# Kernel optimization log

Measured on AMD Instinct MI355X. Metric: run time of the kernel, lower is better.

## Reference

```python
import jax, jax.numpy as jnp
import numpy as np

E, T = 8, 256          # n_experts, chunk length
IN, OUT = 1024, 1024   # input_size, output_size
D1, D2 = 32, 32        # nearest factors of IN
DO1, DO2 = 32, 32      # nearest factors of OUT
B, L = 8, 2048
LOSS_COEF = 1e-5


def setup_inputs() -> dict:
    key = jax.random.key(0)
    ks = jax.random.split(key, 12)
    eyeE = lambda d, k: (jnp.broadcast_to(jnp.eye(d, dtype=jnp.float32), (E, d, d))
                         + 0.01 * jax.random.normal(k, (E, d, d), jnp.float32))
    return {
        "x": jax.random.normal(ks[0], (B, L, IN), jnp.float32),
        "w_gate": 0.02 * jax.random.normal(ks[1], (IN, E), jnp.float32),
        "weight": 0.02 * jax.random.normal(ks[2], (E, OUT, IN), jnp.float32),
        "bias": 0.02 * jax.random.normal(ks[3], (E, OUT), jnp.float32),
        "res_weight": 0.02 * jax.random.normal(ks[4], (OUT, IN), jnp.float32),
        "res_bias": 0.02 * jax.random.normal(ks[5], (1, OUT), jnp.float32),
        "curve1_in": eyeE(D1, ks[6]),
        "curve2_in": eyeE(D2, ks[7]),
        "curve1_out": eyeE(DO1, ks[8]),
        "curve2_out": eyeE(DO2, ks[9]),
        "curve1_bias": eyeE(DO1, ks[10]),
        "curve2_bias": eyeE(DO2, ks[11]),
    }


def _cv_squared(v):
    v = v.astype(jnp.float32)
    return jnp.var(v, ddof=1) / (jnp.mean(v) ** 2 + 1e-10)


def reference(x, w_gate, weight, bias, res_weight, res_bias,
              curve1_in, curve2_in, curve1_out, curve2_out,
              curve1_bias, curve2_bias):
    Bx, Lx, d = x.shape
    N = Lx // T
    BN = Bx * N
    xr = x.reshape(BN, T, d)

    # --- gating (eval mode, ties_merging forces k = n_experts -> plain softmax) ---
    logits = xr.mean(axis=1) @ w_gate            # [BN, E]
    gates = jax.nn.softmax(logits, axis=1)        # [BN, E]
    load = (gates > 0).sum(axis=0).astype(jnp.float32)
    importance = gates.sum(axis=0)
    loss = (_cv_squared(importance) + _cv_squared(load)) * LOSS_COEF

    # --- roll gates by one segment, keeping each sample's first chunk (detached) ---
    e_first = jax.lax.stop_gradient(gates.reshape(Bx, N, E)[:, 0])
    g = jnp.roll(gates, 1, axis=0).reshape(Bx, N, E)
    g = g.at[:, 0].set(e_first).reshape(BN, E)

    # --- Kronecker curve-factored expert weight merge ---
    rw = (weight - res_weight).reshape(E, DO1, DO2, D1, D2)
    rw = jnp.einsum('bij,bjklm->biklm', curve1_out, rw)
    rw = jnp.einsum('bik,bjklm->bjilm', curve2_out, rw)
    rw = jnp.einsum('bil,bjklm->bjkim', curve1_in, rw)
    rw = jnp.einsum('bim,bjklm->bjkli', curve2_in, rw)
    rw = rw.reshape(E, OUT, IN)
    expert_weights = res_weight + jnp.einsum('be,eoi->boi', g, rw)  # [BN, O, I]

    y = jnp.einsum('bij,bkj->bik', xr, expert_weights)  # [BN, T, O]

    # --- curve-factored expert bias merge ---
    rb = (bias - res_bias).reshape(E, DO1, DO2)
    rb = jnp.einsum('bki,bij->bkj', curve1_bias, rb)      # [E, DO1, DO2]
    rb = jnp.einsum('bkj,bij->bik', curve2_bias, rb)      # [E, DO1, DO2]
    rb = rb.reshape(E, OUT)
    expert_bias = res_bias + jnp.einsum('be,eo->bo', g, rb)  # [BN, O]

    y = (y + expert_bias[:, None, :]).reshape(Bx, Lx, OUT)
    return y, loss
```

## Files before the change

kernel.cpp:

```cpp
#include <hip/hip_runtime.h>
#include <cstdint>

typedef __bf16 bf16x8 __attribute__((ext_vector_type(8)));
typedef float  f32x4  __attribute__((ext_vector_type(4)));
typedef unsigned int u32x4 __attribute__((ext_vector_type(4)));
using u16 = unsigned short;

struct alignas(8) u16x4 { u16 x, y, z, w; };

__device__ __forceinline__ u16 f2bf(float f) {
  unsigned u = __builtin_bit_cast(unsigned, f);
  u = (u + 0x7FFFu + ((u >> 16) & 1u)) >> 16;
  return (u16)u;
}
__device__ __forceinline__ float bf2f(u16 u) {
  unsigned v = ((unsigned)u) << 16;
  return __builtin_bit_cast(float, v);
}

static constexpr size_t OFF_XBF  = 0;
static constexpr size_t OFF_EW   = 33554432;
static constexpr size_t OFF_T2   = 33554432;
static constexpr size_t OFF_PM   = 67108864;
static constexpr size_t OFF_RW   = 167772160;
static constexpr size_t OFF_LG   = 201326592;
static constexpr size_t OFF_G    = 201588736;
static constexpr size_t OFF_RB   = 201592832;
static constexpr size_t WS_NEED  = 201887744;

__global__ __launch_bounds__(256) void k_means(const float* __restrict__ x,
                                               float* __restrict__ pm,
                                               u16* __restrict__ xbf) {
  int b = blockIdx.x, q = blockIdx.y, tid = threadIdx.x;
  const float* xb = x + (size_t)b * 262144 + (size_t)q * 16384 + tid * 4;
  u16* xo = xbf + (size_t)b * 262144 + (size_t)q * 16384 + tid * 4;
  float s0 = 0.f, s1 = 0.f, s2 = 0.f, s3 = 0.f;
#pragma unroll
  for (int t = 0; t < 16; ++t) {
    float4 v = *(const float4*)(xb + t * 1024);
    s0 += v.x; s1 += v.y; s2 += v.z; s3 += v.w;
    u16x4 o; o.x = f2bf(v.x); o.y = f2bf(v.y); o.z = f2bf(v.z); o.w = f2bf(v.w);
    *(u16x4*)(xo + t * 1024) = o;
  }
  float4 sv; sv.x = s0; sv.y = s1; sv.z = s2; sv.w = s3;
  *(float4*)(pm + ((size_t)b * 16 + q) * 1024 + tid * 4) = sv;
}

__global__ __launch_bounds__(256) void k_redlogits(const float* __restrict__ pm,
                                                   const float* __restrict__ w_gate,
                                                   float* __restrict__ logits) {
  __shared__ float red[4][8];
  int b = blockIdx.x, tid = threadIdx.x;
  const float* p = pm + (size_t)b * 16384 + tid * 4;
  float4 s = {0.f, 0.f, 0.f, 0.f};
#pragma unroll
  for (int q = 0; q < 16; ++q) {
    float4 v = *(const float4*)(p + q * 1024);
    s.x += v.x; s.y += v.y; s.z += v.z; s.w += v.w;
  }
  int i0 = tid * 4;
  float acc[8];
#pragma unroll
  for (int e = 0; e < 8; ++e) {
    acc[e] = s.x * w_gate[(i0 + 0) * 8 + e] + s.y * w_gate[(i0 + 1) * 8 + e]
           + s.z * w_gate[(i0 + 2) * 8 + e] + s.w * w_gate[(i0 + 3) * 8 + e];
  }
#pragma unroll
  for (int off = 32; off >= 1; off >>= 1)
#pragma unroll
    for (int e = 0; e < 8; ++e) acc[e] += __shfl_down(acc[e], off, 64);
  int wv = tid >> 6;
  if ((tid & 63) == 0)
#pragma unroll
    for (int e = 0; e < 8; ++e) red[wv][e] = acc[e];
  __syncthreads();
  if (tid < 8)
    logits[b * 8 + tid] =
        (red[0][tid] + red[1][tid] + red[2][tid] + red[3][tid]) * (1.f / 256.f);
}

__global__ __launch_bounds__(256) void k_mergeA(const float* __restrict__ W,
                                                const float* __restrict__ R,
                                                const float* __restrict__ c1o,
                                                const float* __restrict__ c2o,
                                                u16* __restrict__ T2t,
                                                const float* __restrict__ bias,
                                                const float* __restrict__ res_bias,
                                                const float* __restrict__ c1b,
                                                const float* __restrict__ c2b,
                                                float* __restrict__ rb) {
  int e = blockIdx.y, bx = blockIdx.x, tid = threadIdx.x;
  if (bx == 128) {
    __shared__ float rb0[32][33], rb1[32][33], m1b[32][32], m2b[32][32];
    for (int idx = tid; idx < 1024; idx += 256) {
      int i = idx >> 5, j = idx & 31;
      rb0[i][j] = bias[e * 1024 + idx] - res_bias[idx];
      m1b[i][j] = c1b[e * 1024 + idx];
      m2b[i][j] = c2b[e * 1024 + idx];
    }
    __syncthreads();
    for (int idx = tid; idx < 1024; idx += 256) {
      int p = idx >> 5, j = idx & 31;
      float s = 0.f;
#pragma unroll
      for (int i = 0; i < 32; ++i) s += m1b[p][i] * rb0[i][j];
      rb1[p][j] = s;
    }
    __syncthreads();
    for (int idx = tid; idx < 1024; idx += 256) {
      int p = idx >> 5, q = idx & 31;
      float s = 0.f;
#pragma unroll
      for (int j = 0; j < 32; ++j) s += m2b[q][j] * rb1[p][j];
      rb[e * 1024 + idx] = s;
    }
    return;
  }
  __shared__ float dw[8 * 1024];
  __shared__ float m1[1024], m2[1024];
  int c0 = bx * 8;
  const float* We = W + (size_t)e * 1048576;
  for (int idx = tid; idx < 1024; idx += 256) {
    m1[idx] = c1o[e * 1024 + idx];
    m2[idx] = c2o[e * 1024 + idx];
  }
  {
    int r = tid >> 1, h = (tid & 1) * 4;
#pragma unroll
    for (int i = 0; i < 8; ++i) {
      int row = r + i * 128;
      const float4 wv = *(const float4*)(We + (size_t)row * 1024 + c0 + h);
      const float4 rv = *(const float4*)(R + (size_t)row * 1024 + c0 + h);
      dw[(h + 0) * 1024 + row] = wv.x - rv.x;
      dw[(h + 1) * 1024 + row] = wv.y - rv.y;
      dw[(h + 2) * 1024 + row] = wv.z - rv.z;
      dw[(h + 3) * 1024 + row] = wv.w - rv.w;
    }
  }
  __syncthreads();
  int i1 = tid & 31, c = tid >> 5;
  const float* dwc = dw + c * 1024;
  float U[32];
#pragma unroll
  for (int k = 0; k < 32; ++k) U[k] = 0.f;
  for (int j = 0; j < 32; ++j) {
    float cj = m1[i1 * 32 + j];
    const float4* rowp = (const float4*)(dwc + j * 32);
#pragma unroll
    for (int k4 = 0; k4 < 8; ++k4) {
      float4 v = rowp[k4];
      U[k4 * 4 + 0] += cj * v.x; U[k4 * 4 + 1] += cj * v.y;
      U[k4 * 4 + 2] += cj * v.z; U[k4 * 4 + 3] += cj * v.w;
    }
  }
  u16* obase = T2t + (size_t)e * 1048576 + (size_t)(c0 + c) * 1024 + i1 * 32;
#pragma unroll
  for (int g4 = 0; g4 < 8; ++g4) {
    float s[4];
#pragma unroll
    for (int q = 0; q < 4; ++q) {
      const float4* m2r = (const float4*)(m2 + (g4 * 4 + q) * 32);
      float acc = 0.f;
#pragma unroll
      for (int k4 = 0; k4 < 8; ++k4) {
        float4 mv = m2r[k4];
        acc += mv.x * U[k4 * 4 + 0] + mv.y * U[k4 * 4 + 1]
             + mv.z * U[k4 * 4 + 2] + mv.w * U[k4 * 4 + 3];
      }
      s[q] = acc;
    }
    u16x4 o4; o4.x = f2bf(s[0]); o4.y = f2bf(s[1]); o4.z = f2bf(s[2]); o4.w = f2bf(s[3]);
    *(u16x4*)(obase + g4 * 4) = o4;
  }
}

__global__ __launch_bounds__(256) void k_mergeB(const u16* __restrict__ T2t,
                                                const float* __restrict__ c1i,
                                                const float* __restrict__ c2i,
                                                const float* __restrict__ R,
                                                u16* __restrict__ RWbf,
                                                const float* __restrict__ logits,
                                                float* __restrict__ g,
                                                float* __restrict__ loss_out) {
  int e = blockIdx.y, bx = blockIdx.x, tid = threadIdx.x;
  if (bx == 128) {
    if (e != 0) return;
    __shared__ float gates[64][8];
    __shared__ float imp[8];
    if (tid < 64) {
      float lg[8];
#pragma unroll
      for (int j = 0; j < 8; ++j) lg[j] = logits[tid * 8 + j];
      float mx = lg[0];
#pragma unroll
      for (int j = 1; j < 8; ++j) mx = fmaxf(mx, lg[j]);
      float s = 0.f, ex[8];
#pragma unroll
      for (int j = 0; j < 8; ++j) { ex[j] = expf(lg[j] - mx); s += ex[j]; }
      float inv = 1.f / s;
#pragma unroll
      for (int j = 0; j < 8; ++j) gates[tid][j] = ex[j] * inv;
    }
    __syncthreads();
    if (tid < 8) {
      float s = 0.f;
      for (int bb = 0; bb < 64; ++bb) s += gates[bb][tid];
      imp[tid] = s;
    }
    __syncthreads();
    if (tid == 0) {
      float mean = 0.f;
#pragma unroll
      for (int j = 0; j < 8; ++j) mean += imp[j];
      mean *= (1.f / 8.f);
      float var = 0.f;
#pragma unroll
      for (int j = 0; j < 8; ++j) { float d = imp[j] - mean; var += d * d; }
      var *= (1.f / 7.f);
      loss_out[0] = (var / (mean * mean + 1e-10f)) * 1e-5f;
    }
    __syncthreads();
    if (tid < 64) {
      int src = ((tid & 7) == 0) ? tid : tid - 1;
#pragma unroll
      for (int j = 0; j < 8; ++j) g[tid * 8 + j] = gates[src][j];
    }
    return;
  }
  __shared__ float t2[8 * 1024];
  __shared__ float m1[1024], m2[1024];
  int o0 = bx * 8;
  const u16* Te = T2t + (size_t)e * 1048576;
  for (int idx = tid; idx < 1024; idx += 256) {
    m1[idx] = c1i[e * 1024 + idx];
    m2[idx] = c2i[e * 1024 + idx];
  }
  {
    int r = tid >> 1, h = (tid & 1) * 4;
#pragma unroll
    for (int i = 0; i < 8; ++i) {
      int row = r + i * 128;
      const u16x4 tv = *(const u16x4*)(Te + (size_t)row * 1024 + o0 + h);
      t2[(h + 0) * 1024 + row] = bf2f(tv.x);
      t2[(h + 1) * 1024 + row] = bf2f(tv.y);
      t2[(h + 2) * 1024 + row] = bf2f(tv.z);
      t2[(h + 3) * 1024 + row] = bf2f(tv.w);
    }
  }
  __syncthreads();
  int i1 = tid & 31, oc = tid >> 5;
  const float* t2c = t2 + oc * 1024;
  float A[32];
#pragma unroll
  for (int m = 0; m < 32; ++m) A[m] = 0.f;
  for (int l = 0; l < 32; ++l) {
    float cl = m1[i1 * 32 + l];
    const float4* rowp = (const float4*)(t2c + l * 32);
#pragma unroll
    for (int m4 = 0; m4 < 8; ++m4) {
      float4 v = rowp[m4];
      A[m4 * 4 + 0] += cl * v.x; A[m4 * 4 + 1] += cl * v.y;
      A[m4 * 4 + 2] += cl * v.z; A[m4 * 4 + 3] += cl * v.w;
    }
  }
  const float* Rrow = R + (size_t)(o0 + oc) * 1024 + i1 * 32;
  u16* obase = RWbf + ((size_t)e * 1024 + o0 + oc) * 1024 + i1 * 32;
#pragma unroll
  for (int g4 = 0; g4 < 8; ++g4) {
    float s[4];
#pragma unroll
    for (int q = 0; q < 4; ++q) {
      const float4* m2r = (const float4*)(m2 + (g4 * 4 + q) * 32);
      float acc = Rrow[g4 * 4 + q];
#pragma unroll
      for (int m4 = 0; m4 < 8; ++m4) {
        float4 mv = m2r[m4];
        acc += mv.x * A[m4 * 4 + 0] + mv.y * A[m4 * 4 + 1]
             + mv.z * A[m4 * 4 + 2] + mv.w * A[m4 * 4 + 3];
      }
      s[q] = acc;
    }
    u16x4 o4; o4.x = f2bf(s[0]); o4.y = f2bf(s[1]); o4.z = f2bf(s[2]); o4.w = f2bf(s[3]);
    *(u16x4*)(obase + g4 * 4) = o4;
  }
}

__global__ __launch_bounds__(256) void k_combine(const u16* __restrict__ RWbf,
                                                 const float* __restrict__ g,
                                                 u16* __restrict__ EW) {
  __shared__ float gs[512];
  int blk = blockIdx.x, tid = threadIdx.x;
  for (int idx = tid; idx < 512; idx += 256) gs[idx] = g[idx];
  __syncthreads();
  int o = blk * 2 + (tid >> 7);
  int i0 = (tid & 127) * 8;
  float w[8][8];
#pragma unroll
  for (int e = 0; e < 8; ++e) {
    u32x4 v = *(const u32x4*)(RWbf + (size_t)e * 1048576 + (size_t)o * 1024 + i0);
#pragma unroll
    for (int h = 0; h < 4; ++h) {
      w[e][2 * h]     = __builtin_bit_cast(float, v[h] << 16);
      w[e][2 * h + 1] = __builtin_bit_cast(float, v[h] & 0xFFFF0000u);
    }
  }
  for (int b = 0; b < 64; ++b) {
    float a[8];
#pragma unroll
    for (int j = 0; j < 8; ++j) a[j] = 0.f;
#pragma unroll
    for (int e = 0; e < 8; ++e) {
      float ge = gs[b * 8 + e];
#pragma unroll
      for (int j = 0; j < 8; ++j) a[j] += ge * w[e][j];
    }
    u32x4 pk;
#pragma unroll
    for (int h = 0; h < 4; ++h)
      pk[h] = (unsigned)f2bf(a[2 * h]) | ((unsigned)f2bf(a[2 * h + 1]) << 16);
    *(u32x4*)(EW + (size_t)b * 1048576 + (size_t)o * 1024 + i0) = pk;
  }
}

__global__ __launch_bounds__(512) void k_gemm(const u16* __restrict__ Xb,
                                              const u16* __restrict__ EW,
                                              const float* __restrict__ rb,
                                              const float* __restrict__ res_b,
                                              const float* __restrict__ g,
                                              float* __restrict__ Y) {
  __shared__ alignas(16) u16 As[2][256 * 64];
  __shared__ alignas(16) u16 Bs[2][256 * 64];
  int hw = blockIdx.x;
  int xcd = hw & 7;
  int b  = xcd * 8 + (hw >> 5);
  int nt = (hw >> 3) & 3;
  int t0 = b * 256, o0 = nt * 256;
  int tid = threadIdx.x, lane = tid & 63, wv = tid >> 6;
  int wr = wv >> 2, wc = wv & 3;
  f32x4 acc[8][4] = {};
  const u16* aG = Xb + (size_t)t0 * 1024;
  const u16* bG = EW + (size_t)b * 1048576 + (size_t)o0 * 1024;
  int srow = tid >> 3;
  int kcol = (tid & 7) << 3;
  int lr = lane & 15;
  int sx = lr & 7;
  u32x4 la[4], lb[4];
#pragma unroll
  for (int iss = 0; iss < 4; ++iss) {
    int r = srow + iss * 64;
    la[iss] = *(const u32x4*)(aG + (size_t)r * 1024 + kcol);
    lb[iss] = *(const u32x4*)(bG + (size_t)r * 1024 + kcol);
  }
  for (int kt = 0; kt < 16; ++kt) {
    int cur = kt & 1;
#pragma unroll
    for (int iss = 0; iss < 4; ++iss) {
      int r = srow + iss * 64;
      int wcl = (((tid & 7) ^ (r & 7)) << 3);
      *(u32x4*)&As[cur][r * 64 + wcl] = la[iss];
      *(u32x4*)&Bs[cur][r * 64 + wcl] = lb[iss];
    }
    __syncthreads();
    if (kt < 15) {
      int k0n = (kt + 1) << 6;
#pragma unroll
      for (int iss = 0; iss < 4; ++iss) {
        int r = srow + iss * 64;
        la[iss] = *(const u32x4*)(aG + (size_t)r * 1024 + k0n + kcol);
        lb[iss] = *(const u32x4*)(bG + (size_t)r * 1024 + k0n + kcol);
      }
    }
#pragma unroll
    for (int kk = 0; kk < 2; ++kk) {
      int c16 = kk * 4 + (lane >> 4);
      int cp = ((c16 ^ sx) << 3);
      bf16x8 af[8], bfr[4];
#pragma unroll
      for (int mi = 0; mi < 8; ++mi)
        af[mi] = *(const bf16x8*)&As[cur][(wr * 128 + mi * 16 + lr) * 64 + cp];
#pragma unroll
      for (int ni = 0; ni < 4; ++ni)
        bfr[ni] = *(const bf16x8*)&Bs[cur][(wc * 64 + ni * 16 + lr) * 64 + cp];
#pragma unroll
      for (int mi = 0; mi < 8; ++mi)
#pragma unroll
        for (int ni = 0; ni < 4; ++ni)
          acc[mi][ni] = __builtin_amdgcn_mfma_f32_16x16x32_bf16(af[mi], bfr[ni], acc[mi][ni], 0, 0, 0);
    }
  }
  float ge[8];
#pragma unroll
  for (int e = 0; e < 8; ++e) ge[e] = g[b * 8 + e];
  int rbase = (lane >> 4) << 2;
#pragma unroll
  for (int ni = 0; ni < 4; ++ni) {
    int o = o0 + wc * 64 + ni * 16 + lr;
    float ebv = res_b[o];
#pragma unroll
    for (int e = 0; e < 8; ++e) ebv += ge[e] * rb[e * 1024 + o];
#pragma unroll
    for (int mi = 0; mi < 8; ++mi) {
      int trow = t0 + wr * 128 + mi * 16 + rbase;
      float* yp = Y + (size_t)trow * 1024 + o;
      yp[0]    = acc[mi][ni][0] + ebv;
      yp[1024] = acc[mi][ni][1] + ebv;
      yp[2048] = acc[mi][ni][2] + ebv;
      yp[3072] = acc[mi][ni][3] + ebv;
    }
  }
}

extern "C" void kernel_launch(void* const* d_in, const int* in_sizes, int n_in,
                              void* d_out, int out_size, void* d_ws, size_t ws_size,
                              hipStream_t stream) {
  const float* x      = (const float*)d_in[0];
  const float* w_gate = (const float*)d_in[1];
  const float* weight = (const float*)d_in[2];
  const float* bias   = (const float*)d_in[3];
  const float* res_w  = (const float*)d_in[4];
  const float* res_b  = (const float*)d_in[5];
  const float* c1i    = (const float*)d_in[6];
  const float* c2i    = (const float*)d_in[7];
  const float* c1o    = (const float*)d_in[8];
  const float* c2o    = (const float*)d_in[9];
  const float* c1b    = (const float*)d_in[10];
  const float* c2b    = (const float*)d_in[11];
  float* y = (float*)d_out;

  if (ws_size < WS_NEED) return;

  char* wsb = (char*)d_ws;
  u16*   xbf   = (u16*)(wsb + OFF_XBF);
  u16*   EW    = (u16*)(wsb + OFF_EW);
  u16*   T2t   = (u16*)(wsb + OFF_T2);
  float* pm    = (float*)(wsb + OFF_PM);
  u16*   RWbf  = (u16*)(wsb + OFF_RW);
  float* lgts  = (float*)(wsb + OFF_LG);
  float* g     = (float*)(wsb + OFF_G);
  float* rb    = (float*)(wsb + OFF_RB);

  k_means    <<<dim3(64, 16), 256, 0, stream>>>(x, pm, xbf);
  k_redlogits<<<64, 256, 0, stream>>>(pm, w_gate, lgts);
  k_mergeA   <<<dim3(129, 8), 256, 0, stream>>>(weight, res_w, c1o, c2o, T2t,
                                                bias, res_b, c1b, c2b, rb);
  k_mergeB   <<<dim3(129, 8), 256, 0, stream>>>(T2t, c1i, c2i, res_w, RWbf,
                                                lgts, g, y + 16777216);
  k_combine  <<<512, 256, 0, stream>>>(RWbf, g, EW);
  k_gemm     <<<256, 512, 0, stream>>>(xbf, EW, rb, res_b, g, y);
}
```

Before: 205.4 us.

## Use direct global-to-LDS async loads with smaller 256x128 GEMM tiles

```diff
diff --git a/kernel.cpp b/kernel.cpp
--- a/kernel.cpp
+++ b/kernel.cpp
@@ -17,6 +17,10 @@
   unsigned v = ((unsigned)u) << 16;
   return __builtin_bit_cast(float, v);
 }
+
+#define ASYNC16(gp, lp) __builtin_amdgcn_global_load_lds( \
+    (__attribute__((address_space(1))) void*)(void*)(gp),  \
+    (__attribute__((address_space(3))) void*)(lp), 16, 0, 0)
 
 static constexpr size_t OFF_XBF  = 0;
 static constexpr size_t OFF_EW   = 33554432;
@@ -328,65 +332,54 @@
                                               const float* __restrict__ res_b,
                                               const float* __restrict__ g,
                                               float* __restrict__ Y) {
-  __shared__ alignas(16) u16 As[2][256 * 64];
-  __shared__ alignas(16) u16 Bs[2][256 * 64];
+  __shared__ alignas(16) u16 As[256 * 64];
+  __shared__ alignas(16) u16 Bs[128 * 64];
   int hw = blockIdx.x;
   int xcd = hw & 7;
-  int b  = xcd * 8 + (hw >> 5);
-  int nt = (hw >> 3) & 3;
-  int t0 = b * 256, o0 = nt * 256;
+  int b  = xcd * 8 + (hw >> 6);
+  int nt = (hw >> 3) & 7;
+  int t0 = b * 256, o0 = nt * 128;
   int tid = threadIdx.x, lane = tid & 63, wv = tid >> 6;
-  int wr = wv >> 2, wc = wv & 3;
-  f32x4 acc[8][4] = {};
+  int wr = wv >> 1, wc = wv & 1;
+  f32x4 acc[4][4] = {};
   const u16* aG = Xb + (size_t)t0 * 1024;
   const u16* bG = EW + (size_t)b * 1048576 + (size_t)o0 * 1024;
   int srow = tid >> 3;
-  int kcol = (tid & 7) << 3;
+  int scol = (tid & 7) << 3;
+  int gcol = (((tid & 7) ^ (srow & 7)) << 3);
   int lr = lane & 15;
   int sx = lr & 7;
-  u32x4 la[4], lb[4];
-#pragma unroll
-  for (int iss = 0; iss < 4; ++iss) {
-    int r = srow + iss * 64;
-    la[iss] = *(const u32x4*)(aG + (size_t)r * 1024 + kcol);
-    lb[iss] = *(const u32x4*)(bG + (size_t)r * 1024 + kcol);
-  }
   for (int kt = 0; kt < 16; ++kt) {
-    int cur = kt & 1;
+    int k0 = kt << 6;
 #pragma unroll
     for (int iss = 0; iss < 4; ++iss) {
       int r = srow + iss * 64;
-      int wcl = (((tid & 7) ^ (r & 7)) << 3);
-      *(u32x4*)&As[cur][r * 64 + wcl] = la[iss];
-      *(u32x4*)&Bs[cur][r * 64 + wcl] = lb[iss];
-    }
-    __syncthreads();
-    if (kt < 15) {
-      int k0n = (kt + 1) << 6;
-#pragma unroll
-      for (int iss = 0; iss < 4; ++iss) {
-        int r = srow + iss * 64;
-        la[iss] = *(const u32x4*)(aG + (size_t)r * 1024 + k0n + kcol);
-        lb[iss] = *(const u32x4*)(bG + (size_t)r * 1024 + k0n + kcol);
-      }
-    }
+      ASYNC16(aG + (size_t)r * 1024 + k0 + gcol, &As[r * 64 + scol]);
+    }
+#pragma unroll
+    for (int iss = 0; iss < 2; ++iss) {
+      int r = srow + iss * 64;
+      ASYNC16(bG + (size_t)r * 1024 + k0 + gcol, &Bs[r * 64 + scol]);
+    }
+    __syncthreads();
 #pragma unroll
     for (int kk = 0; kk < 2; ++kk) {
       int c16 = kk * 4 + (lane >> 4);
       int cp = ((c16 ^ sx) << 3);
-      bf16x8 af[8], bfr[4];
-#pragma unroll
-      for (int mi = 0; mi < 8; ++mi)
-        af[mi] = *(const bf16x8*)&As[cur][(wr * 128 + mi * 16 + lr) * 64 + cp];
+      bf16x8 af[4], bfr[4];
+#pragma unroll
+      for (int mi = 0; mi < 4; ++mi)
+        af[mi] = *(const bf16x8*)&As[(wr * 64 + mi * 16 + lr) * 64 + cp];
 #pragma unroll
       for (int ni = 0; ni < 4; ++ni)
-        bfr[ni] = *(const bf16x8*)&Bs[cur][(wc * 64 + ni * 16 + lr) * 64 + cp];
-#pragma unroll
-      for (int mi = 0; mi < 8; ++mi)
+        bfr[ni] = *(const bf16x8*)&Bs[(wc * 64 + ni * 16 + lr) * 64 + cp];
+#pragma unroll
+      for (int mi = 0; mi < 4; ++mi)
 #pragma unroll
         for (int ni = 0; ni < 4; ++ni)
           acc[mi][ni] = __builtin_amdgcn_mfma_f32_16x16x32_bf16(af[mi], bfr[ni], acc[mi][ni], 0, 0, 0);
     }
+    __syncthreads();
   }
   float ge[8];
 #pragma unroll
@@ -399,8 +392,8 @@
 #pragma unroll
     for (int e = 0; e < 8; ++e) ebv += ge[e] * rb[e * 1024 + o];
 #pragma unroll
-    for (int mi = 0; mi < 8; ++mi) {
-      int trow = t0 + wr * 128 + mi * 16 + rbase;
+    for (int mi = 0; mi < 4; ++mi) {
+      int trow = t0 + wr * 64 + mi * 16 + rbase;
       float* yp = Y + (size_t)trow * 1024 + o;
       yp[0]    = acc[mi][ni][0] + ebv;
       yp[1024] = acc[mi][ni][1] + ebv;
@@ -446,5 +439,5 @@
   k_mergeB   <<<dim3(129, 8), 256, 0, stream>>>(T2t, c1i, c2i, res_w, RWbf,
                                                 lgts, g, y + 16777216);
   k_combine  <<<512, 256, 0, stream>>>(RWbf, g, EW);
-  k_gemm     <<<256, 512, 0, stream>>>(xbf, EW, rb, res_b, g, y);
-}
+  k_gemm     <<<512, 512, 0, stream>>>(xbf, EW, rb, res_b, g, y);
+}
```

After: 210.7 us. 2.6% more time.
